# Kernel tuning notes

Hardware: AMD Instinct MI355X
Metric: run time of the kernel (lower is better)

Reference implementation:

```python
import jax, jax.numpy as jnp
import numpy as np

TAU = 2.0
V_TH = 1.0


def setup_inputs() -> dict:
    key = jax.random.key(0)
    k1, k2, k3 = jax.random.split(key, 3)
    T, B, N = 128, 64, 1024
    x = jax.random.normal(k1, (T, B, N), dtype=jnp.float32)
    # nn.Linear(hidden, hidden, bias=False) weights: [out, in]
    scale = 1.0 / np.sqrt(N)
    W1 = jax.random.uniform(k2, (N, N), dtype=jnp.float32, minval=-scale, maxval=scale)
    W2 = jax.random.uniform(k3, (N, N), dtype=jnp.float32, minval=-scale, maxval=scale)
    return {"x": x, "W1": W1, "W2": W2}


def _lif_scan(h_seq):
    # h_seq: [T, B, N]; LIF recurrence with tau=2, v_th=1, reset v = h*(1-s)
    def step(v, x_t):
        h = v + (x_t - v) / TAU
        s = (h >= V_TH).astype(h.dtype)
        return h * (1.0 - s), s

    v0 = jnp.zeros(h_seq.shape[1:], dtype=h_seq.dtype)
    _, spikes = jax.lax.scan(step, v0, h_seq)
    return spikes  # [T, B, N]


def reference(x, W1, W2):
    # fc1: y = x @ W1^T (torch Linear convention)
    h = jnp.einsum('tbn,mn->tbm', x, W1)
    spike = _lif_scan(h)
    return jnp.einsum('tbn,mn->tbm', spike, W2)
```

## Files before the change

kernel.cpp:

```cpp
#include <hip/hip_runtime.h>
#include <hip/hip_bf16.h>
#include <stdint.h>


#define TT 128
#define BB 64
#define NN 1024
#define MROWS (TT * BB)
#define SROW  (BB * NN)
#define MiB   ((size_t)1048576)

typedef _Float16 h8  __attribute__((ext_vector_type(8)));
typedef _Float16 h4v __attribute__((ext_vector_type(4)));
typedef float    f4  __attribute__((ext_vector_type(4)));
typedef float    v2f __attribute__((ext_vector_type(2)));

#if __has_builtin(__builtin_elementwise_fma)
#define V2FMA(a, b, c) __builtin_elementwise_fma((a), (b), (c))
#else
static __device__ __forceinline__ v2f v2fma_(v2f a, v2f b, v2f c) {
    v2f r; r[0] = fmaf(a[0], b[0], c[0]); r[1] = fmaf(a[1], b[1], c[1]); return r;
}
#define V2FMA(a, b, c) v2fma_((a), (b), (c))
#endif

#define GL2LDS(g, l) __builtin_amdgcn_global_load_lds(                         \
    (const __attribute__((address_space(1))) void*)(const void*)(g),           \
    (__attribute__((address_space(3))) void*)(void*)(l), 16, 0, 0)

__global__ __launch_bounds__(256) void prep(const float* __restrict__ x,
                                            const float* __restrict__ W1,
                                            const float* __restrict__ W2,
                                            _Float16* __restrict__ A0, _Float16* __restrict__ A1,
                                            _Float16* __restrict__ B0, _Float16* __restrict__ B1,
                                            float* __restrict__ W2T) {
    const int nb = blockIdx.x;
    const int tid = threadIdx.x;
    if (nb < 8192 + 1024) {
        const bool isX = nb < 8192;
        const float* src = isX ? x : W1;
        _Float16* d0 = isX ? A0 : B0;
        _Float16* d1 = isX ? A1 : B1;
        const int i = (isX ? nb : nb - 8192) * 256 + tid;
        const float4 v = reinterpret_cast<const float4*>(src)[i];
        const float f[4] = {v.x, v.y, v.z, v.w};
        h4v a0, a1;
#pragma unroll
        for (int j = 0; j < 4; ++j) {
            const _Float16 c = (_Float16)f[j];
            a0[j] = c;
            a1[j] = (_Float16)((f[j] - (float)c) * 4096.0f);
        }
        reinterpret_cast<h4v*>(d0)[i] = a0;
        reinterpret_cast<h4v*>(d1)[i] = a1;
    } else {
        __shared__ float tile[32][33];
        const int tIdx = nb - 9216;
        const int bx = (tIdx & 31) * 32, by = (tIdx >> 5) * 32;
        const int tx = tid & 31, ty = tid >> 5;
#pragma unroll
        for (int j = 0; j < 32; j += 8)
            tile[ty + j][tx] = W2[(size_t)(by + ty + j) * NN + bx + tx];
        __syncthreads();
#pragma unroll
        for (int j = 0; j < 32; j += 8)
            W2T[(size_t)(bx + ty + j) * NN + by + tx] = tile[tx][ty + j];
    }
}

__global__ __launch_bounds__(256, 2) void gemm_split(const _Float16* __restrict__ A0,
                                                     const _Float16* __restrict__ A1,
                                                     const _Float16* __restrict__ B0,
                                                     const _Float16* __restrict__ B1,
                                                     float* __restrict__ C) {
    __shared__ _Float16 As0[2][4096], As1[2][4096], Bs0[2][4096], Bs1[2][4096];
    const int tid  = threadIdx.x;
    const int lane = tid & 63;
    const int wid  = tid >> 6;
    const int wr   = wid >> 1, wc = wid & 1;
    const int rowBase = blockIdx.y * 128;
    const int colBase = blockIdx.x * 128;

    const int srow = wid * 32 + (lane >> 2);
    const int swz  = (((lane & 3) ^ ((srow >> 1) & 3)) << 3);
    const size_t aOff0 = (size_t)(rowBase + srow) * NN + swz;
    const size_t aOff1 = aOff0 + (size_t)16 * NN;
    const size_t bOff0 = (size_t)(colBase + srow) * NN + swz;
    const size_t bOff1 = bOff0 + (size_t)16 * NN;
    const int ldsB0 = wid * 1024;
    const int ldsB1 = wid * 1024 + 512;

    int fA[4], fB[4];
#pragma unroll
    for (int i = 0; i < 4; ++i) {
        const int ra = wr * 64 + i * 16 + (lane & 15);
        const int rb = wc * 64 + i * 16 + (lane & 15);
        fA[i] = ra * 32 + (((lane >> 4) ^ ((ra >> 1) & 3)) << 3);
        fB[i] = rb * 32 + (((lane >> 4) ^ ((rb >> 1) & 3)) << 3);
    }

    f4 acc0[4][4], acc1[4][4];
#pragma unroll
    for (int i = 0; i < 4; ++i)
#pragma unroll
        for (int j = 0; j < 4; ++j) { acc0[i][j] = (f4)0.0f; acc1[i][j] = (f4)0.0f; }

#define STAGE(bi, K0)                                     \
    do {                                                  \
        GL2LDS(A0 + aOff0 + (K0), &As0[bi][ldsB0]);       \
        GL2LDS(A0 + aOff1 + (K0), &As0[bi][ldsB1]);       \
        GL2LDS(A1 + aOff0 + (K0), &As1[bi][ldsB0]);       \
        GL2LDS(A1 + aOff1 + (K0), &As1[bi][ldsB1]);       \
        GL2LDS(B0 + bOff0 + (K0), &Bs0[bi][ldsB0]);       \
        GL2LDS(B0 + bOff1 + (K0), &Bs0[bi][ldsB1]);       \
        GL2LDS(B1 + bOff0 + (K0), &Bs1[bi][ldsB0]);       \
        GL2LDS(B1 + bOff1 + (K0), &Bs1[bi][ldsB1]);       \
    } while (0)

    STAGE(0, 0);
    __syncthreads();

    const int NT = NN / 32;
    for (int t = 0; t < NT; ++t) {
        const int cur = t & 1;
        if (t < NT - 1) STAGE(cur ^ 1, (t + 1) * 32);
        h8 a0f[4], a1f[4], b0f[4], b1f[4];
#pragma unroll
        for (int i = 0; i < 4; ++i) {
            a0f[i] = *(const h8*)&As0[cur][fA[i]];
            a1f[i] = *(const h8*)&As1[cur][fA[i]];
            b0f[i] = *(const h8*)&Bs0[cur][fB[i]];
            b1f[i] = *(const h8*)&Bs1[cur][fB[i]];
        }
#pragma unroll
        for (int i = 0; i < 4; ++i)
#pragma unroll
            for (int j = 0; j < 4; ++j) {
                acc0[i][j] = __builtin_amdgcn_mfma_f32_16x16x32_f16(a0f[i], b0f[j], acc0[i][j], 0, 0, 0);
                acc1[i][j] = __builtin_amdgcn_mfma_f32_16x16x32_f16(a0f[i], b1f[j], acc1[i][j], 0, 0, 0);
                acc1[i][j] = __builtin_amdgcn_mfma_f32_16x16x32_f16(a1f[i], b0f[j], acc1[i][j], 0, 0, 0);
            }
        __syncthreads();
    }
#undef STAGE

    const int orow = rowBase + wr * 64 + (lane >> 4) * 4;
    const int ocol = colBase + wc * 64 + (lane & 15);
#pragma unroll
    for (int i = 0; i < 4; ++i)
#pragma unroll
        for (int j = 0; j < 4; ++j)
#pragma unroll
            for (int q = 0; q < 4; ++q)
                C[(size_t)(orow + i * 16 + q) * NN + ocol + j * 16] =
                    acc0[i][j][q] + acc1[i][j][q] * (1.0f / 4096.0f);
}

__global__ __launch_bounds__(256) void lif_scan(const float* __restrict__ H,
                                                unsigned long long* __restrict__ mask) {
    const int g = blockIdx.x * 256 + threadIdx.x;
    const int b = g >> 10;
    const int n = g & 1023;
    const int word = n >> 6;
    const bool lane0 = (threadIdx.x & 63) == 0;

    float v = 0.0f;
    float buf[8];
#pragma unroll
    for (int j = 0; j < 8; ++j) buf[j] = H[(size_t)j * SROW + g];

    for (int t0 = 0; t0 < TT; t0 += 8) {
        float nbuf[8];
        if (t0 + 8 < TT) {
#pragma unroll
            for (int j = 0; j < 8; ++j) nbuf[j] = H[(size_t)(t0 + 8 + j) * SROW + g];
        } else {
#pragma unroll
            for (int j = 0; j < 8; ++j) nbuf[j] = 0.f;
        }
#pragma unroll
        for (int j = 0; j < 8; ++j) {
            const float x = buf[j];
            const float h = v + (x - v) * 0.5f;
            const bool s = (h >= 1.0f);
            v = s ? 0.0f : h;
            const unsigned long long m = __ballot(s);
            if (lane0) mask[((size_t)(t0 + j) * BB + b) * 16 + word] = m;
        }
#pragma unroll
        for (int j = 0; j < 8; ++j) buf[j] = nbuf[j];
    }
}

__global__ __launch_bounds__(256) void spike_matmul(const unsigned long long* __restrict__ mask,
                                                    const float* __restrict__ W2T,
                                                    float* __restrict__ out) {
    __shared__ unsigned long long sw[16];
    const int r = blockIdx.x;
    const int tid = threadIdx.x;
    if (tid < 16) sw[tid] = mask[(size_t)r * 16 + tid];
    __syncthreads();

    f4 acc = (f4)0.0f;
#pragma unroll 1
    for (int w = 0; w < 16; ++w) {
        unsigned long long bits = sw[w];
        while (bits) {
            const int n = w * 64 + (__ffsll(bits) - 1);
            bits &= bits - 1;
            const f4 rv = reinterpret_cast<const f4*>(W2T + (size_t)n * NN)[tid];
            acc[0] += rv[0]; acc[1] += rv[1]; acc[2] += rv[2]; acc[3] += rv[3];
        }
    }
    reinterpret_cast<f4*>(out + (size_t)r * NN)[tid] = acc;
}

__global__ __launch_bounds__(256) void transpose_nn(const float* __restrict__ in,
                                                    float* __restrict__ out) {
    __shared__ float tile[32][33];
    const int bx = blockIdx.x * 32, by = blockIdx.y * 32;
    const int tx = threadIdx.x, ty = threadIdx.y;
#pragma unroll
    for (int j = 0; j < 32; j += 8)
        tile[ty + j][tx] = in[(size_t)(by + ty + j) * NN + bx + tx];
    __syncthreads();
#pragma unroll
    for (int j = 0; j < 32; j += 8)
        out[(size_t)(bx + ty + j) * NN + by + tx] = tile[tx][ty + j];
}

#define BM 128
#define BN 64
#define BK 16
__global__ __launch_bounds__(256, 4) void gemm1_f32(const float* __restrict__ A,
                                                    const float* __restrict__ B,
                                                    float* __restrict__ C) {
    __shared__ float Asb[2][BK][132];
    __shared__ float Bsb[2][BK][68];
    const int tid = threadIdx.x;
    const int ty = tid >> 4;
    const int tx = tid & 15;
    const int rowBase = blockIdx.y * BM;
    const int colBase = blockIdx.x * BN;
    const int sr = tid >> 2;
    const int sk = (tid & 3) * 4;

    const float* Ap0 = A + (size_t)(rowBase + sr) * NN + sk;
    const float* Ap1 = Ap0 + (size_t)64 * NN;
    const float* Bp  = B + (size_t)(colBase + sr) * NN + sk;

    v2f acc[4][4];
#pragma unroll
    for (int i = 0; i < 4; ++i)
#pragma unroll
        for (int j = 0; j < 4; ++j) acc[i][j] = (v2f){0.f, 0.f};

    float4 ra0 = *(const float4*)Ap0;
    float4 ra1 = *(const float4*)Ap1;
    float4 rb  = *(const float4*)Bp;

#define STW(buf)                                                                       \
    do {                                                                               \
        Asb[buf][sk + 0][sr] = ra0.x; Asb[buf][sk + 1][sr] = ra0.y;                    \
        Asb[buf][sk + 2][sr] = ra0.z; Asb[buf][sk + 3][sr] = ra0.w;                    \
        Asb[buf][sk + 0][sr + 64] = ra1.x; Asb[buf][sk + 1][sr + 64] = ra1.y;          \
        Asb[buf][sk + 2][sr + 64] = ra1.z; Asb[buf][sk + 3][sr + 64] = ra1.w;          \
        Bsb[buf][sk + 0][sr] = rb.x;  Bsb[buf][sk + 1][sr] = rb.y;                     \
        Bsb[buf][sk + 2][sr] = rb.z;  Bsb[buf][sk + 3][sr] = rb.w;                     \
    } while (0)

    STW(0);
    __syncthreads();
    const int NT = NN / BK;
    for (int t = 0; t < NT; ++t) {
        const int cur = t & 1;
        if (t < NT - 1) {
            const int ko = (t + 1) * BK;
            ra0 = *(const float4*)(Ap0 + ko);
            ra1 = *(const float4*)(Ap1 + ko);
            rb  = *(const float4*)(Bp + ko);
        }
#pragma unroll
        for (int k = 0; k < BK; ++k) {
            const v2f* ap = (const v2f*)&Asb[cur][k][ty * 8];
            const float4 bf = *(const float4*)&Bsb[cur][k][tx * 4];
            const float bb[4] = {bf.x, bf.y, bf.z, bf.w};
            const v2f a0 = ap[0], a1 = ap[1], a2 = ap[2], a3 = ap[3];
#pragma unroll
            for (int j = 0; j < 4; ++j) {
                const v2f bd = {bb[j], bb[j]};
                acc[0][j] = V2FMA(a0, bd, acc[0][j]);
                acc[1][j] = V2FMA(a1, bd, acc[1][j]);
                acc[2][j] = V2FMA(a2, bd, acc[2][j]);
                acc[3][j] = V2FMA(a3, bd, acc[3][j]);
            }
        }
        if (t < NT - 1) STW(cur ^ 1);
        __syncthreads();
    }
#undef STW
    float* Cp = C + (size_t)(rowBase + ty * 8) * NN + colBase + tx * 4;
#pragma unroll
    for (int rp = 0; rp < 4; ++rp) {
        float4 lo = {acc[rp][0][0], acc[rp][1][0], acc[rp][2][0], acc[rp][3][0]};
        float4 hi = {acc[rp][0][1], acc[rp][1][1], acc[rp][2][1], acc[rp][3][1]};
        *(float4*)(Cp + (size_t)(2 * rp) * NN)     = lo;
        *(float4*)(Cp + (size_t)(2 * rp + 1) * NN) = hi;
    }
}

extern "C" void kernel_launch(void* const* d_in, const int* in_sizes, int n_in,
                              void* d_out, int out_size, void* d_ws, size_t ws_size,
                              hipStream_t stream) {
    const float* x  = (const float*)d_in[0];
    const float* W1 = (const float*)d_in[1];
    const float* W2 = (const float*)d_in[2];
    float* out = (float*)d_out;

    unsigned long long* mask = (unsigned long long*)d_ws;
    float* W2T = (float*)((char*)d_ws + 1 * MiB);

    if (ws_size >= 43 * MiB) {
        _Float16* A0 = (_Float16*)((char*)d_ws + 5 * MiB);
        _Float16* A1 = (_Float16*)((char*)d_ws + 22 * MiB);
        _Float16* B0 = (_Float16*)((char*)d_ws + 39 * MiB);
        _Float16* B1 = (_Float16*)((char*)d_ws + 41 * MiB);

        prep<<<8192 + 1024 + 1024, 256, 0, stream>>>(x, W1, W2, A0, A1, B0, B1, W2T);
        gemm_split<<<dim3(NN / 128, MROWS / 128), 256, 0, stream>>>(A0, A1, B0, B1, out);
    } else {
        transpose_nn<<<dim3(32, 32), dim3(32, 8), 0, stream>>>(W2, W2T);
        gemm1_f32<<<dim3(NN / BN, MROWS / BM), 256, 0, stream>>>(x, W1, out);
    }
    lif_scan<<<SROW / 256, 256, 0, stream>>>(out, mask);
    spike_matmul<<<MROWS, 256, 0, stream>>>(mask, W2T, out);
}
```

Baseline: 181.3 us.

## Fuse x fp16 hi/lo split into GEMM, drop A pre-pass, remap blocks

The prep kernel no longer converts x into two fp16 arrays. The GEMM now stages raw fp32 x tiles into LDS with a swizzle and does the hi/lo fp16 split in registers right before the MFMAs, which removes a full read/write pass over the 32 MB input. Blocks are remapped to a 1D grid with grouped row/column ordering for better L2 reuse of W1. The LIF scan prefetch depth also grows from 8 to 16 timesteps. The trade-off is more ALU work and doubled A-tile LDS traffic inside the GEMM inner loop.

```diff
diff --git a/kernel.cpp b/kernel.cpp
--- a/kernel.cpp
+++ b/kernel.cpp
@@ -28,21 +28,15 @@
     (const __attribute__((address_space(1))) void*)(const void*)(g),           \
     (__attribute__((address_space(3))) void*)(void*)(l), 16, 0, 0)
 
-__global__ __launch_bounds__(256) void prep(const float* __restrict__ x,
-                                            const float* __restrict__ W1,
+__global__ __launch_bounds__(256) void prep(const float* __restrict__ W1,
                                             const float* __restrict__ W2,
-                                            _Float16* __restrict__ A0, _Float16* __restrict__ A1,
                                             _Float16* __restrict__ B0, _Float16* __restrict__ B1,
                                             float* __restrict__ W2T) {
     const int nb = blockIdx.x;
     const int tid = threadIdx.x;
-    if (nb < 8192 + 1024) {
-        const bool isX = nb < 8192;
-        const float* src = isX ? x : W1;
-        _Float16* d0 = isX ? A0 : B0;
-        _Float16* d1 = isX ? A1 : B1;
-        const int i = (isX ? nb : nb - 8192) * 256 + tid;
-        const float4 v = reinterpret_cast<const float4*>(src)[i];
+    if (nb < 1024) {
+        const int i = nb * 256 + tid;
+        const float4 v = reinterpret_cast<const float4*>(W1)[i];
         const float f[4] = {v.x, v.y, v.z, v.w};
         h4v a0, a1;
 #pragma unroll
@@ -51,11 +45,11 @@
             a0[j] = c;
             a1[j] = (_Float16)((f[j] - (float)c) * 4096.0f);
         }
-        reinterpret_cast<h4v*>(d0)[i] = a0;
-        reinterpret_cast<h4v*>(d1)[i] = a1;
+        reinterpret_cast<h4v*>(B0)[i] = a0;
+        reinterpret_cast<h4v*>(B1)[i] = a1;
     } else {
         __shared__ float tile[32][33];
-        const int tIdx = nb - 9216;
+        const int tIdx = nb - 1024;
         const int bx = (tIdx & 31) * 32, by = (tIdx >> 5) * 32;
         const int tx = tid & 31, ty = tid >> 5;
 #pragma unroll
@@ -68,35 +62,41 @@
     }
 }
 
-__global__ __launch_bounds__(256, 2) void gemm_split(const _Float16* __restrict__ A0,
-                                                     const _Float16* __restrict__ A1,
-                                                     const _Float16* __restrict__ B0,
-                                                     const _Float16* __restrict__ B1,
+__global__ __launch_bounds__(256, 2) void gemm_split(const float* __restrict__ X,
+                                                     const _Float16* __restrict__ B0g,
+                                                     const _Float16* __restrict__ B1g,
                                                      float* __restrict__ C) {
-    __shared__ _Float16 As0[2][4096], As1[2][4096], Bs0[2][4096], Bs1[2][4096];
+    __shared__ float    As[2][4096];
+    __shared__ _Float16 Bs0[2][4096], Bs1[2][4096];
     const int tid  = threadIdx.x;
     const int lane = tid & 63;
     const int wid  = tid >> 6;
     const int wr   = wid >> 1, wc = wid & 1;
-    const int rowBase = blockIdx.y * 128;
-    const int colBase = blockIdx.x * 128;
-
-    const int srow = wid * 32 + (lane >> 2);
-    const int swz  = (((lane & 3) ^ ((srow >> 1) & 3)) << 3);
-    const size_t aOff0 = (size_t)(rowBase + srow) * NN + swz;
-    const size_t aOff1 = aOff0 + (size_t)16 * NN;
-    const size_t bOff0 = (size_t)(colBase + srow) * NN + swz;
-    const size_t bOff1 = bOff0 + (size_t)16 * NN;
-    const int ldsB0 = wid * 1024;
-    const int ldsB1 = wid * 1024 + 512;
-
-    int fA[4], fB[4];
+
+    const int ib = blockIdx.x;
+    const int p  = ((ib >> 6) << 3) + (ib & 7);
+    const int cc = (ib >> 3) & 7;
+    const int rowBase = p * 128;
+    const int colBase = cc * 128;
+
+    const size_t aOff = (size_t)(rowBase + wid * 32 + (lane >> 3)) * NN
+                      + (((lane & 7) ^ (lane >> 3)) << 2);
+    const int ldsA = wid * 1024;
+
+    const int srowB = wid * 32 + (lane >> 2);
+    const size_t bOff = (size_t)(colBase + srowB) * NN
+                      + (((lane & 3) ^ ((srowB >> 1) & 3)) << 3);
+    const int ldsB = wid * 1024;
+
+    int fA0[4], fA1[4], fB[4];
 #pragma unroll
     for (int i = 0; i < 4; ++i) {
         const int ra = wr * 64 + i * 16 + (lane & 15);
         const int rb = wc * 64 + i * 16 + (lane & 15);
-        fA[i] = ra * 32 + (((lane >> 4) ^ ((ra >> 1) & 3)) << 3);
-        fB[i] = rb * 32 + (((lane >> 4) ^ ((rb >> 1) & 3)) << 3);
+        const int ca = (lane >> 4) * 2;
+        fA0[i] = ra * 32 + (((ca + 0) ^ (ra & 7)) << 2);
+        fA1[i] = ra * 32 + (((ca + 1) ^ (ra & 7)) << 2);
+        fB[i]  = rb * 32 + (((lane >> 4) ^ ((rb >> 1) & 3)) << 3);
     }
 
     f4 acc0[4][4], acc1[4][4];
@@ -105,16 +105,16 @@
 #pragma unroll
         for (int j = 0; j < 4; ++j) { acc0[i][j] = (f4)0.0f; acc1[i][j] = (f4)0.0f; }
 
-#define STAGE(bi, K0)                                     \
-    do {                                                  \
-        GL2LDS(A0 + aOff0 + (K0), &As0[bi][ldsB0]);       \
-        GL2LDS(A0 + aOff1 + (K0), &As0[bi][ldsB1]);       \
-        GL2LDS(A1 + aOff0 + (K0), &As1[bi][ldsB0]);       \
-        GL2LDS(A1 + aOff1 + (K0), &As1[bi][ldsB1]);       \
-        GL2LDS(B0 + bOff0 + (K0), &Bs0[bi][ldsB0]);       \
-        GL2LDS(B0 + bOff1 + (K0), &Bs0[bi][ldsB1]);       \
-        GL2LDS(B1 + bOff0 + (K0), &Bs1[bi][ldsB0]);       \
-        GL2LDS(B1 + bOff1 + (K0), &Bs1[bi][ldsB1]);       \
+#define STAGE(bi, K0)                                              \
+    do {                                                           \
+        GL2LDS(X + aOff + (size_t)0  * NN + (K0), &As[bi][ldsA]);          \
+        GL2LDS(X + aOff + (size_t)8  * NN + (K0), &As[bi][ldsA + 256]);    \
+        GL2LDS(X + aOff + (size_t)16 * NN + (K0), &As[bi][ldsA + 512]);    \
+        GL2LDS(X + aOff + (size_t)24 * NN + (K0), &As[bi][ldsA + 768]);    \
+        GL2LDS(B0g + bOff + (K0),                  &Bs0[bi][ldsB]);        \
+        GL2LDS(B0g + bOff + (size_t)16 * NN + (K0), &Bs0[bi][ldsB + 512]); \
+        GL2LDS(B1g + bOff + (K0),                  &Bs1[bi][ldsB]);        \
+        GL2LDS(B1g + bOff + (size_t)16 * NN + (K0), &Bs1[bi][ldsB + 512]); \
     } while (0)
 
     STAGE(0, 0);
@@ -124,11 +124,21 @@
     for (int t = 0; t < NT; ++t) {
         const int cur = t & 1;
         if (t < NT - 1) STAGE(cur ^ 1, (t + 1) * 32);
+
         h8 a0f[4], a1f[4], b0f[4], b1f[4];
 #pragma unroll
         for (int i = 0; i < 4; ++i) {
-            a0f[i] = *(const h8*)&As0[cur][fA[i]];
-            a1f[i] = *(const h8*)&As1[cur][fA[i]];
+            const f4 lo = *(const f4*)&As[cur][fA0[i]];
+            const f4 hi = *(const f4*)&As[cur][fA1[i]];
+#pragma unroll
+            for (int e = 0; e < 4; ++e) {
+                const float fl = lo[e], fh = hi[e];
+                const _Float16 cl = (_Float16)fl, ch = (_Float16)fh;
+                a0f[i][e]     = cl;
+                a0f[i][4 + e] = ch;
+                a1f[i][e]     = (_Float16)((fl - (float)cl) * 4096.0f);
+                a1f[i][4 + e] = (_Float16)((fh - (float)ch) * 4096.0f);
+            }
             b0f[i] = *(const h8*)&Bs0[cur][fB[i]];
             b1f[i] = *(const h8*)&Bs1[cur][fB[i]];
         }
@@ -165,21 +175,21 @@
     const bool lane0 = (threadIdx.x & 63) == 0;
 
     float v = 0.0f;
-    float buf[8];
-#pragma unroll
-    for (int j = 0; j < 8; ++j) buf[j] = H[(size_t)j * SROW + g];
-
-    for (int t0 = 0; t0 < TT; t0 += 8) {
-        float nbuf[8];
-        if (t0 + 8 < TT) {
-#pragma unroll
-            for (int j = 0; j < 8; ++j) nbuf[j] = H[(size_t)(t0 + 8 + j) * SROW + g];
+    float buf[16];
+#pragma unroll
+    for (int j = 0; j < 16; ++j) buf[j] = H[(size_t)j * SROW + g];
+
+    for (int t0 = 0; t0 < TT; t0 += 16) {
+        float nbuf[16];
+        if (t0 + 16 < TT) {
+#pragma unroll
+            for (int j = 0; j < 16; ++j) nbuf[j] = H[(size_t)(t0 + 16 + j) * SROW + g];
         } else {
 #pragma unroll
-            for (int j = 0; j < 8; ++j) nbuf[j] = 0.f;
-        }
-#pragma unroll
-        for (int j = 0; j < 8; ++j) {
+            for (int j = 0; j < 16; ++j) nbuf[j] = 0.f;
+        }
+#pragma unroll
+        for (int j = 0; j < 16; ++j) {
             const float x = buf[j];
             const float h = v + (x - v) * 0.5f;
             const bool s = (h >= 1.0f);
@@ -188,7 +198,7 @@
             if (lane0) mask[((size_t)(t0 + j) * BB + b) * 16 + word] = m;
         }
 #pragma unroll
-        for (int j = 0; j < 8; ++j) buf[j] = nbuf[j];
+        for (int j = 0; j < 16; ++j) buf[j] = nbuf[j];
     }
 }
 
@@ -320,14 +330,12 @@
     unsigned long long* mask = (unsigned long long*)d_ws;
     float* W2T = (float*)((char*)d_ws + 1 * MiB);
 
-    if (ws_size >= 43 * MiB) {
-        _Float16* A0 = (_Float16*)((char*)d_ws + 5 * MiB);
-        _Float16* A1 = (_Float16*)((char*)d_ws + 22 * MiB);
-        _Float16* B0 = (_Float16*)((char*)d_ws + 39 * MiB);
-        _Float16* B1 = (_Float16*)((char*)d_ws + 41 * MiB);
-
-        prep<<<8192 + 1024 + 1024, 256, 0, stream>>>(x, W1, W2, A0, A1, B0, B1, W2T);
-        gemm_split<<<dim3(NN / 128, MROWS / 128), 256, 0, stream>>>(A0, A1, B0, B1, out);
+    if (ws_size >= 9 * MiB) {
+        _Float16* B0 = (_Float16*)((char*)d_ws + 5 * MiB);
+        _Float16* B1 = (_Float16*)((char*)d_ws + 7 * MiB);
+
+        prep<<<2048, 256, 0, stream>>>(W1, W2, B0, B1, W2T);
+        gemm_split<<<512, 256, 0, stream>>>(x, B0, B1, out);
     } else {
         transpose_nn<<<dim3(32, 32), dim3(32, 8), 0, stream>>>(W2, W2T);
         gemm1_f32<<<dim3(NN / BN, MROWS / BM), 256, 0, stream>>>(x, W1, out);
```

Measured after the change: 179.4 us. No clear change (-1.0%).

## Fuse prep, GEMM, LIF scan and spike matmul into one cooperative persistent kernel

Applied to the files above, without the earlier changes.

Replaces the four separate launches with a single cooperative kernel of 512 blocks that runs the split/transpose prep, the fp16-split MFMA GEMM, the LIF scan and the spike matmul as phases separated by grid.sync. This removes per-launch overhead and the gaps between kernels. It also remaps GEMM tiles to a grouped order for L2 reuse, halves the scan's active threads while deepening its prefetch to 16 steps, and makes each spike-matmul block handle 16 rows. In exchange, each phase is limited to 512 blocks, which lowers parallelism in prep and scan, and grid-wide barriers add cost. If the cooperative launch fails, the code falls back to four separate kernels, and the fp32 fallback path for small workspaces is dropped.

```diff
diff --git a/kernel.cpp b/kernel.cpp
--- a/kernel.cpp
+++ b/kernel.cpp
@@ -1,6 +1,9 @@
 #include <hip/hip_runtime.h>
+#include <hip/hip_cooperative_groups.h>
 #include <hip/hip_bf16.h>
 #include <stdint.h>
+
+namespace cg = cooperative_groups;
 
 
 #define TT 128
@@ -13,73 +16,57 @@
 typedef _Float16 h8  __attribute__((ext_vector_type(8)));
 typedef _Float16 h4v __attribute__((ext_vector_type(4)));
 typedef float    f4  __attribute__((ext_vector_type(4)));
-typedef float    v2f __attribute__((ext_vector_type(2)));
-
-#if __has_builtin(__builtin_elementwise_fma)
-#define V2FMA(a, b, c) __builtin_elementwise_fma((a), (b), (c))
-#else
-static __device__ __forceinline__ v2f v2fma_(v2f a, v2f b, v2f c) {
-    v2f r; r[0] = fmaf(a[0], b[0], c[0]); r[1] = fmaf(a[1], b[1], c[1]); return r;
-}
-#define V2FMA(a, b, c) v2fma_((a), (b), (c))
-#endif
 
 #define GL2LDS(g, l) __builtin_amdgcn_global_load_lds(                         \
     (const __attribute__((address_space(1))) void*)(const void*)(g),           \
     (__attribute__((address_space(3))) void*)(void*)(l), 16, 0, 0)
 
-__global__ __launch_bounds__(256) void prep(const float* __restrict__ x,
-                                            const float* __restrict__ W1,
-                                            const float* __restrict__ W2,
-                                            _Float16* __restrict__ A0, _Float16* __restrict__ A1,
-                                            _Float16* __restrict__ B0, _Float16* __restrict__ B1,
-                                            float* __restrict__ W2T) {
-    const int nb = blockIdx.x;
-    const int tid = threadIdx.x;
-    if (nb < 8192 + 1024) {
-        const bool isX = nb < 8192;
-        const float* src = isX ? x : W1;
-        _Float16* d0 = isX ? A0 : B0;
-        _Float16* d1 = isX ? A1 : B1;
-        const int i = (isX ? nb : nb - 8192) * 256 + tid;
-        const float4 v = reinterpret_cast<const float4*>(src)[i];
-        const float f[4] = {v.x, v.y, v.z, v.w};
-        h4v a0, a1;
-#pragma unroll
-        for (int j = 0; j < 4; ++j) {
-            const _Float16 c = (_Float16)f[j];
-            a0[j] = c;
-            a1[j] = (_Float16)((f[j] - (float)c) * 4096.0f);
-        }
-        reinterpret_cast<h4v*>(d0)[i] = a0;
-        reinterpret_cast<h4v*>(d1)[i] = a1;
-    } else {
-        __shared__ float tile[32][33];
-        const int tIdx = nb - 9216;
-        const int bx = (tIdx & 31) * 32, by = (tIdx >> 5) * 32;
-        const int tx = tid & 31, ty = tid >> 5;
-#pragma unroll
-        for (int j = 0; j < 32; j += 8)
-            tile[ty + j][tx] = W2[(size_t)(by + ty + j) * NN + bx + tx];
-        __syncthreads();
-#pragma unroll
-        for (int j = 0; j < 32; j += 8)
-            W2T[(size_t)(bx + ty + j) * NN + by + tx] = tile[tx][ty + j];
-    }
-}
-
-__global__ __launch_bounds__(256, 2) void gemm_split(const _Float16* __restrict__ A0,
-                                                     const _Float16* __restrict__ A1,
-                                                     const _Float16* __restrict__ B0,
-                                                     const _Float16* __restrict__ B1,
-                                                     float* __restrict__ C) {
-    __shared__ _Float16 As0[2][4096], As1[2][4096], Bs0[2][4096], Bs1[2][4096];
-    const int tid  = threadIdx.x;
-    const int lane = tid & 63;
-    const int wid  = tid >> 6;
-    const int wr   = wid >> 1, wc = wid & 1;
-    const int rowBase = blockIdx.y * 128;
-    const int colBase = blockIdx.x * 128;
+
+__device__ __forceinline__ void dev_split4(const float* __restrict__ src,
+                                           _Float16* __restrict__ d0,
+                                           _Float16* __restrict__ d1, int i) {
+    const float4 v = reinterpret_cast<const float4*>(src)[i];
+    const float f[4] = {v.x, v.y, v.z, v.w};
+    h4v a0, a1;
+#pragma unroll
+    for (int j = 0; j < 4; ++j) {
+        const _Float16 c = (_Float16)f[j];
+        a0[j] = c;
+        a1[j] = (_Float16)((f[j] - (float)c) * 4096.0f);
+    }
+    reinterpret_cast<h4v*>(d0)[i] = a0;
+    reinterpret_cast<h4v*>(d1)[i] = a1;
+}
+
+__device__ __forceinline__ void dev_transpose(int tIdx, int tid, const float* __restrict__ in,
+                                              float* __restrict__ outp, float* tile ) {
+    const int bx = (tIdx & 31) * 32, by = (tIdx >> 5) * 32;
+    const int tx = tid & 31, ty = tid >> 5;
+#pragma unroll
+    for (int j = 0; j < 32; j += 8)
+        tile[(ty + j) * 33 + tx] = in[(size_t)(by + ty + j) * NN + bx + tx];
+    __syncthreads();
+#pragma unroll
+    for (int j = 0; j < 32; j += 8)
+        outp[(size_t)(bx + ty + j) * NN + by + tx] = tile[tx * 33 + ty + j];
+    __syncthreads();
+}
+
+__device__ __forceinline__ void dev_gemm(int ib, int tid, unsigned char* smem,
+                                         const _Float16* __restrict__ A0,
+                                         const _Float16* __restrict__ A1,
+                                         const _Float16* __restrict__ B0,
+                                         const _Float16* __restrict__ B1,
+                                         float* __restrict__ C) {
+    _Float16* As0 = (_Float16*)smem;
+    _Float16* As1 = (_Float16*)(smem + 16384);
+    _Float16* Bs0 = (_Float16*)(smem + 32768);
+    _Float16* Bs1 = (_Float16*)(smem + 49152);
+    const int lane = tid & 63, wid = tid >> 6;
+    const int wr = wid >> 1, wc = wid & 1;
+    const int p  = ((ib >> 6) << 3) + (ib & 7);
+    const int cc = (ib >> 3) & 7;
+    const int rowBase = p * 128, colBase = cc * 128;
 
     const int srow = wid * 32 + (lane >> 2);
     const int swz  = (((lane & 3) ^ ((srow >> 1) & 3)) << 3);
@@ -87,8 +74,7 @@
     const size_t aOff1 = aOff0 + (size_t)16 * NN;
     const size_t bOff0 = (size_t)(colBase + srow) * NN + swz;
     const size_t bOff1 = bOff0 + (size_t)16 * NN;
-    const int ldsB0 = wid * 1024;
-    const int ldsB1 = wid * 1024 + 512;
+    const int l0 = wid * 1024, l1 = wid * 1024 + 512;
 
     int fA[4], fB[4];
 #pragma unroll
@@ -105,32 +91,31 @@
 #pragma unroll
         for (int j = 0; j < 4; ++j) { acc0[i][j] = (f4)0.0f; acc1[i][j] = (f4)0.0f; }
 
-#define STAGE(bi, K0)                                     \
-    do {                                                  \
-        GL2LDS(A0 + aOff0 + (K0), &As0[bi][ldsB0]);       \
-        GL2LDS(A0 + aOff1 + (K0), &As0[bi][ldsB1]);       \
-        GL2LDS(A1 + aOff0 + (K0), &As1[bi][ldsB0]);       \
-        GL2LDS(A1 + aOff1 + (K0), &As1[bi][ldsB1]);       \
-        GL2LDS(B0 + bOff0 + (K0), &Bs0[bi][ldsB0]);       \
-        GL2LDS(B0 + bOff1 + (K0), &Bs0[bi][ldsB1]);       \
-        GL2LDS(B1 + bOff0 + (K0), &Bs1[bi][ldsB0]);       \
-        GL2LDS(B1 + bOff1 + (K0), &Bs1[bi][ldsB1]);       \
+#define STAGE(bi, K0)                                            \
+    do {                                                         \
+        GL2LDS(A0 + aOff0 + (K0), &As0[(bi) * 4096 + l0]);       \
+        GL2LDS(A0 + aOff1 + (K0), &As0[(bi) * 4096 + l1]);       \
+        GL2LDS(A1 + aOff0 + (K0), &As1[(bi) * 4096 + l0]);       \
+        GL2LDS(A1 + aOff1 + (K0), &As1[(bi) * 4096 + l1]);       \
+        GL2LDS(B0 + bOff0 + (K0), &Bs0[(bi) * 4096 + l0]);       \
+        GL2LDS(B0 + bOff1 + (K0), &Bs0[(bi) * 4096 + l1]);       \
+        GL2LDS(B1 + bOff0 + (K0), &Bs1[(bi) * 4096 + l0]);       \
+        GL2LDS(B1 + bOff1 + (K0), &Bs1[(bi) * 4096 + l1]);       \
     } while (0)
 
     STAGE(0, 0);
     __syncthreads();
 
-    const int NT = NN / 32;
-    for (int t = 0; t < NT; ++t) {
+    for (int t = 0; t < 32; ++t) {
         const int cur = t & 1;
-        if (t < NT - 1) STAGE(cur ^ 1, (t + 1) * 32);
+        if (t < 31) STAGE(cur ^ 1, (t + 1) * 32);
         h8 a0f[4], a1f[4], b0f[4], b1f[4];
 #pragma unroll
         for (int i = 0; i < 4; ++i) {
-            a0f[i] = *(const h8*)&As0[cur][fA[i]];
-            a1f[i] = *(const h8*)&As1[cur][fA[i]];
-            b0f[i] = *(const h8*)&Bs0[cur][fB[i]];
-            b1f[i] = *(const h8*)&Bs1[cur][fB[i]];
+            a0f[i] = *(const h8*)&As0[cur * 4096 + fA[i]];
+            a1f[i] = *(const h8*)&As1[cur * 4096 + fA[i]];
+            b0f[i] = *(const h8*)&Bs0[cur * 4096 + fB[i]];
+            b1f[i] = *(const h8*)&Bs1[cur * 4096 + fB[i]];
         }
 #pragma unroll
         for (int i = 0; i < 4; ++i)
@@ -156,30 +141,25 @@
                     acc0[i][j][q] + acc1[i][j][q] * (1.0f / 4096.0f);
 }
 
-__global__ __launch_bounds__(256) void lif_scan(const float* __restrict__ H,
-                                                unsigned long long* __restrict__ mask) {
-    const int g = blockIdx.x * 256 + threadIdx.x;
-    const int b = g >> 10;
-    const int n = g & 1023;
-    const int word = n >> 6;
-    const bool lane0 = (threadIdx.x & 63) == 0;
-
+__device__ __forceinline__ void dev_scan(int c, const float* __restrict__ H,
+                                         unsigned long long* __restrict__ mask, int tid) {
+    const int b = c >> 10, n = c & 1023, word = n >> 6;
+    const bool lane0 = (tid & 63) == 0;
     float v = 0.0f;
-    float buf[8];
-#pragma unroll
-    for (int j = 0; j < 8; ++j) buf[j] = H[(size_t)j * SROW + g];
-
-    for (int t0 = 0; t0 < TT; t0 += 8) {
-        float nbuf[8];
-        if (t0 + 8 < TT) {
-#pragma unroll
-            for (int j = 0; j < 8; ++j) nbuf[j] = H[(size_t)(t0 + 8 + j) * SROW + g];
+    float buf[16];
+#pragma unroll
+    for (int j = 0; j < 16; ++j) buf[j] = H[(size_t)j * SROW + c];
+    for (int t0 = 0; t0 < TT; t0 += 16) {
+        float nbuf[16];
+        if (t0 + 16 < TT) {
+#pragma unroll
+            for (int j = 0; j < 16; ++j) nbuf[j] = H[(size_t)(t0 + 16 + j) * SROW + c];
         } else {
 #pragma unroll
-            for (int j = 0; j < 8; ++j) nbuf[j] = 0.f;
-        }
-#pragma unroll
-        for (int j = 0; j < 8; ++j) {
+            for (int j = 0; j < 16; ++j) nbuf[j] = 0.f;
+        }
+#pragma unroll
+        for (int j = 0; j < 16; ++j) {
             const float x = buf[j];
             const float h = v + (x - v) * 0.5f;
             const bool s = (h >= 1.0f);
@@ -188,125 +168,100 @@
             if (lane0) mask[((size_t)(t0 + j) * BB + b) * 16 + word] = m;
         }
 #pragma unroll
-        for (int j = 0; j < 8; ++j) buf[j] = nbuf[j];
-    }
-}
-
-__global__ __launch_bounds__(256) void spike_matmul(const unsigned long long* __restrict__ mask,
-                                                    const float* __restrict__ W2T,
-                                                    float* __restrict__ out) {
-    __shared__ unsigned long long sw[16];
-    const int r = blockIdx.x;
-    const int tid = threadIdx.x;
-    if (tid < 16) sw[tid] = mask[(size_t)r * 16 + tid];
-    __syncthreads();
-
-    f4 acc = (f4)0.0f;
+        for (int j = 0; j < 16; ++j) buf[j] = nbuf[j];
+    }
+}
+
+__device__ __forceinline__ void dev_spmm16(int blk, int tid,
+                                           const unsigned long long* __restrict__ mask,
+                                           const float* __restrict__ W2T,
+                                           float* __restrict__ outp,
+                                           unsigned long long* sw ) {
+    sw[tid] = mask[(size_t)blk * 256 + tid];
+    __syncthreads();
 #pragma unroll 1
-    for (int w = 0; w < 16; ++w) {
-        unsigned long long bits = sw[w];
-        while (bits) {
-            const int n = w * 64 + (__ffsll(bits) - 1);
-            bits &= bits - 1;
-            const f4 rv = reinterpret_cast<const f4*>(W2T + (size_t)n * NN)[tid];
-            acc[0] += rv[0]; acc[1] += rv[1]; acc[2] += rv[2]; acc[3] += rv[3];
-        }
-    }
-    reinterpret_cast<f4*>(out + (size_t)r * NN)[tid] = acc;
-}
-
-__global__ __launch_bounds__(256) void transpose_nn(const float* __restrict__ in,
-                                                    float* __restrict__ out) {
-    __shared__ float tile[32][33];
-    const int bx = blockIdx.x * 32, by = blockIdx.y * 32;
-    const int tx = threadIdx.x, ty = threadIdx.y;
-#pragma unroll
-    for (int j = 0; j < 32; j += 8)
-        tile[ty + j][tx] = in[(size_t)(by + ty + j) * NN + bx + tx];
-    __syncthreads();
-#pragma unroll
-    for (int j = 0; j < 32; j += 8)
-        out[(size_t)(bx + ty + j) * NN + by + tx] = tile[tx][ty + j];
-}
-
-#define BM 128
-#define BN 64
-#define BK 16
-__global__ __launch_bounds__(256, 4) void gemm1_f32(const float* __restrict__ A,
-                                                    const float* __restrict__ B,
-                                                    float* __restrict__ C) {
-    __shared__ float Asb[2][BK][132];
-    __shared__ float Bsb[2][BK][68];
-    const int tid = threadIdx.x;
-    const int ty = tid >> 4;
-    const int tx = tid & 15;
-    const int rowBase = blockIdx.y * BM;
-    const int colBase = blockIdx.x * BN;
-    const int sr = tid >> 2;
-    const int sk = (tid & 3) * 4;
-
-    const float* Ap0 = A + (size_t)(rowBase + sr) * NN + sk;
-    const float* Ap1 = Ap0 + (size_t)64 * NN;
-    const float* Bp  = B + (size_t)(colBase + sr) * NN + sk;
-
-    v2f acc[4][4];
-#pragma unroll
-    for (int i = 0; i < 4; ++i)
-#pragma unroll
-        for (int j = 0; j < 4; ++j) acc[i][j] = (v2f){0.f, 0.f};
-
-    float4 ra0 = *(const float4*)Ap0;
-    float4 ra1 = *(const float4*)Ap1;
-    float4 rb  = *(const float4*)Bp;
-
-#define STW(buf)                                                                       \
-    do {                                                                               \
-        Asb[buf][sk + 0][sr] = ra0.x; Asb[buf][sk + 1][sr] = ra0.y;                    \
-        Asb[buf][sk + 2][sr] = ra0.z; Asb[buf][sk + 3][sr] = ra0.w;                    \
-        Asb[buf][sk + 0][sr + 64] = ra1.x; Asb[buf][sk + 1][sr + 64] = ra1.y;          \
-        Asb[buf][sk + 2][sr + 64] = ra1.z; Asb[buf][sk + 3][sr + 64] = ra1.w;          \
-        Bsb[buf][sk + 0][sr] = rb.x;  Bsb[buf][sk + 1][sr] = rb.y;                     \
-        Bsb[buf][sk + 2][sr] = rb.z;  Bsb[buf][sk + 3][sr] = rb.w;                     \
-    } while (0)
-
-    STW(0);
-    __syncthreads();
-    const int NT = NN / BK;
-    for (int t = 0; t < NT; ++t) {
-        const int cur = t & 1;
-        if (t < NT - 1) {
-            const int ko = (t + 1) * BK;
-            ra0 = *(const float4*)(Ap0 + ko);
-            ra1 = *(const float4*)(Ap1 + ko);
-            rb  = *(const float4*)(Bp + ko);
-        }
-#pragma unroll
-        for (int k = 0; k < BK; ++k) {
-            const v2f* ap = (const v2f*)&Asb[cur][k][ty * 8];
-            const float4 bf = *(const float4*)&Bsb[cur][k][tx * 4];
-            const float bb[4] = {bf.x, bf.y, bf.z, bf.w};
-            const v2f a0 = ap[0], a1 = ap[1], a2 = ap[2], a3 = ap[3];
-#pragma unroll
-            for (int j = 0; j < 4; ++j) {
-                const v2f bd = {bb[j], bb[j]};
-                acc[0][j] = V2FMA(a0, bd, acc[0][j]);
-                acc[1][j] = V2FMA(a1, bd, acc[1][j]);
-                acc[2][j] = V2FMA(a2, bd, acc[2][j]);
-                acc[3][j] = V2FMA(a3, bd, acc[3][j]);
+    for (int rr = 0; rr < 16; ++rr) {
+        const int r = blk * 16 + rr;
+        f4 acc = (f4)0.0f;
+#pragma unroll 1
+        for (int w = 0; w < 16; ++w) {
+            unsigned long long bits = sw[rr * 16 + w];
+            while (bits) {
+                const int n2 = w * 64 + (__ffsll(bits) - 1);
+                bits &= bits - 1;
+                const f4 rv = reinterpret_cast<const f4*>(W2T + (size_t)n2 * NN)[tid];
+                acc[0] += rv[0]; acc[1] += rv[1]; acc[2] += rv[2]; acc[3] += rv[3];
             }
         }
-        if (t < NT - 1) STW(cur ^ 1);
-        __syncthreads();
-    }
-#undef STW
-    float* Cp = C + (size_t)(rowBase + ty * 8) * NN + colBase + tx * 4;
-#pragma unroll
-    for (int rp = 0; rp < 4; ++rp) {
-        float4 lo = {acc[rp][0][0], acc[rp][1][0], acc[rp][2][0], acc[rp][3][0]};
-        float4 hi = {acc[rp][0][1], acc[rp][1][1], acc[rp][2][1], acc[rp][3][1]};
-        *(float4*)(Cp + (size_t)(2 * rp) * NN)     = lo;
-        *(float4*)(Cp + (size_t)(2 * rp + 1) * NN) = hi;
-    }
+        reinterpret_cast<f4*>(outp + (size_t)r * NN)[tid] = acc;
+    }
+}
+
+__global__ __launch_bounds__(256, 2) void fused(const float* __restrict__ x,
+                                                const float* __restrict__ W1,
+                                                const float* __restrict__ W2,
+                                                float* __restrict__ out,
+                                                unsigned long long* __restrict__ mask,
+                                                _Float16* __restrict__ A0, _Float16* __restrict__ A1,
+                                                _Float16* __restrict__ B0, _Float16* __restrict__ B1,
+                                                float* __restrict__ W2T) {
+    __shared__ __align__(16) unsigned char smem[65536];
+    const int tid = threadIdx.x, blk = blockIdx.x;
+    cg::grid_group grid = cg::this_grid();
+
+#pragma unroll 1
+    for (int it = 0; it < 20; ++it) {
+        const int vb = blk * 20 + it;
+        if (vb < 8192)       dev_split4(x, A0, A1, vb * 256 + tid);
+        else if (vb < 9216)  dev_split4(W1, B0, B1, (vb - 8192) * 256 + tid);
+        else                 dev_transpose(vb - 9216, tid, W2, W2T, (float*)smem);
+    }
+    __threadfence();
+    grid.sync();
+
+    dev_gemm(blk, tid, smem, A0, A1, B0, B1, out);
+    __threadfence();
+    grid.sync();
+
+    if (tid < 128) dev_scan(blk * 128 + tid, out, mask, tid);
+    __threadfence();
+    grid.sync();
+
+    dev_spmm16(blk, tid, mask, W2T, out, (unsigned long long*)smem);
+}
+
+__global__ __launch_bounds__(256) void k_prep(const float* __restrict__ x,
+                                              const float* __restrict__ W1,
+                                              const float* __restrict__ W2,
+                                              _Float16* __restrict__ A0, _Float16* __restrict__ A1,
+                                              _Float16* __restrict__ B0, _Float16* __restrict__ B1,
+                                              float* __restrict__ W2T) {
+    __shared__ float tile[32 * 33];
+    const int vb = blockIdx.x, tid = threadIdx.x;
+    if (vb < 8192)       dev_split4(x, A0, A1, vb * 256 + tid);
+    else if (vb < 9216)  dev_split4(W1, B0, B1, (vb - 8192) * 256 + tid);
+    else                 dev_transpose(vb - 9216, tid, W2, W2T, tile);
+}
+
+__global__ __launch_bounds__(256, 2) void k_gemm(const _Float16* __restrict__ A0,
+                                                 const _Float16* __restrict__ A1,
+                                                 const _Float16* __restrict__ B0,
+                                                 const _Float16* __restrict__ B1,
+                                                 float* __restrict__ C) {
+    __shared__ __align__(16) unsigned char smem[65536];
+    dev_gemm(blockIdx.x, threadIdx.x, smem, A0, A1, B0, B1, C);
+}
+
+__global__ __launch_bounds__(256) void k_scan(const float* __restrict__ H,
+                                              unsigned long long* __restrict__ mask) {
+    if (threadIdx.x < 128) dev_scan(blockIdx.x * 128 + threadIdx.x, H, mask, threadIdx.x);
+}
+
+__global__ __launch_bounds__(256) void k_spmm(const unsigned long long* __restrict__ mask,
+                                              const float* __restrict__ W2T,
+                                              float* __restrict__ outp) {
+    __shared__ unsigned long long sw[256];
+    dev_spmm16(blockIdx.x, threadIdx.x, mask, W2T, outp, sw);
 }
 
 extern "C" void kernel_launch(void* const* d_in, const int* in_sizes, int n_in,
@@ -318,20 +273,20 @@
     float* out = (float*)d_out;
 
     unsigned long long* mask = (unsigned long long*)d_ws;
-    float* W2T = (float*)((char*)d_ws + 1 * MiB);
-
-    if (ws_size >= 43 * MiB) {
-        _Float16* A0 = (_Float16*)((char*)d_ws + 5 * MiB);
-        _Float16* A1 = (_Float16*)((char*)d_ws + 22 * MiB);
-        _Float16* B0 = (_Float16*)((char*)d_ws + 39 * MiB);
-        _Float16* B1 = (_Float16*)((char*)d_ws + 41 * MiB);
-
-        prep<<<8192 + 1024 + 1024, 256, 0, stream>>>(x, W1, W2, A0, A1, B0, B1, W2T);
-        gemm_split<<<dim3(NN / 128, MROWS / 128), 256, 0, stream>>>(A0, A1, B0, B1, out);
-    } else {
-        transpose_nn<<<dim3(32, 32), dim3(32, 8), 0, stream>>>(W2, W2T);
-        gemm1_f32<<<dim3(NN / BN, MROWS / BM), 256, 0, stream>>>(x, W1, out);
-    }
-    lif_scan<<<SROW / 256, 256, 0, stream>>>(out, mask);
-    spike_matmul<<<MROWS, 256, 0, stream>>>(mask, W2T, out);
-}
+    float* W2T   = (float*)((char*)d_ws + 1 * MiB);
+    _Float16* A0 = (_Float16*)((char*)d_ws + 5 * MiB);
+    _Float16* A1 = (_Float16*)((char*)d_ws + 22 * MiB);
+    _Float16* B0 = (_Float16*)((char*)d_ws + 39 * MiB);
+    _Float16* B1 = (_Float16*)((char*)d_ws + 41 * MiB);
+
+    void* kargs[] = {(void*)&x, (void*)&W1, (void*)&W2, (void*)&out, (void*)&mask,
+                     (void*)&A0, (void*)&A1, (void*)&B0, (void*)&B1, (void*)&W2T};
+    hipError_t err = hipLaunchCooperativeKernel((void*)fused, dim3(512), dim3(256),
+                                                kargs, 0, stream);
+    if (err != hipSuccess) {
+        k_prep<<<10240, 256, 0, stream>>>(x, W1, W2, A0, A1, B0, B1, W2T);
+        k_gemm<<<512, 256, 0, stream>>>(A0, A1, B0, B1, out);
+        k_scan<<<512, 256, 0, stream>>>(out, mask);
+        k_spmm<<<512, 256, 0, stream>>>(mask, W2T, out);
+    }
+}
```

Result: slower. 545.8 us (+201.1%).
